# Kernel optimization log

Hardware: AMD Instinct MI355X
Metric: run time of the kernel (lower is better)

## Reference

```python
import jax, jax.numpy as jnp
import numpy as np

NEG_SLOPE = 0.2
HEADS = 8

def _gat_conv(x, src, dst, n_nodes, W, att_src, att_dst, bias):
    # x: [N, Fin], W: [Fin, H*C], att_*: [H, C], bias: [C]
    H, C = att_src.shape
    xl = (x @ W).reshape(n_nodes, H, C)                      # [N,H,C]
    a_src = (xl * att_src[None]).sum(-1)                      # [N,H]
    a_dst = (xl * att_dst[None]).sum(-1)                      # [N,H]
    e = jax.nn.leaky_relu(a_src[src] + a_dst[dst], NEG_SLOPE) # [E,H]
    m = jax.ops.segment_max(e, dst, num_segments=n_nodes)     # [N,H]
    ee = jnp.exp(e - m[dst])
    s = jax.ops.segment_sum(ee, dst, num_segments=n_nodes)    # [N,H]
    alpha = ee / s[dst]                                       # [E,H]
    msg = alpha[:, :, None] * xl[src]                         # [E,H,C]
    out = jax.ops.segment_sum(msg, dst, num_segments=n_nodes) # [N,H,C]
    return out.mean(axis=1) + bias                            # [N,C] (concat=False)

def setup_inputs() -> dict:
    key = jax.random.key(0)
    ks = jax.random.split(key, 12)
    N, E, EL = 50000, 800000, 200000
    V, D, HID, OUT = 5000, 128, 32, 32
    inp = {}
    inp['x'] = jax.random.randint(ks[0], (N,), 0, V)
    inp['edge_index'] = jax.random.randint(ks[1], (2, E), 0, N)
    inp['edge_label_index'] = jax.random.randint(ks[2], (2, EL), 0, N)
    inp['emb'] = jax.random.normal(ks[3], (V, D), jnp.float32) * D ** -0.5
    inp['W1'] = jax.random.normal(ks[4], (D, HEADS * HID), jnp.float32) * D ** -0.5
    inp['att_src1'] = jax.random.normal(ks[5], (HEADS, HID), jnp.float32) * HID ** -0.5
    inp['att_dst1'] = jax.random.normal(ks[6], (HEADS, HID), jnp.float32) * HID ** -0.5
    inp['b1'] = jnp.zeros((HID,), jnp.float32)
    inp['W2'] = jax.random.normal(ks[7], (HID, HEADS * OUT), jnp.float32) * HID ** -0.5
    inp['att_src2'] = jax.random.normal(ks[8], (HEADS, OUT), jnp.float32) * OUT ** -0.5
    inp['att_dst2'] = jax.random.normal(ks[9], (HEADS, OUT), jnp.float32) * OUT ** -0.5
    inp['b2'] = jnp.zeros((OUT,), jnp.float32)
    return inp

def reference(x, edge_index, edge_label_index, emb, W1, att_src1, att_dst1, b1, W2, att_src2, att_dst2, b2):
    N = x.shape[0]
    # PyG GATConv adds self-loops by default
    loop = jnp.arange(N)
    src = jnp.concatenate([edge_index[0], loop])
    dst = jnp.concatenate([edge_index[1], loop])
    h = emb[x]                                                   # [N, D] embedding lookup (squeeze(1) equivalent)
    h = jax.nn.relu(_gat_conv(h, src, dst, N, W1, att_src1, att_dst1, b1))
    # dropout p=0.5 is identity at inference (training=False)
    z = _gat_conv(h, src, dst, N, W2, att_src2, att_dst2, b2)    # [N, OUT]
    # decode: dot product over label edges
    return (z[edge_label_index[0]] * z[edge_label_index[1]]).sum(axis=-1)
```

## Files before the change

### kernel.cpp

```cpp
#include <hip/hip_runtime.h>
#include <hip/hip_fp16.h>
#include <math.h>
#include <limits.h>

#define HH 8
#define CC 32
#define NEG 0.2f

struct __align__(8) half4 { __half2 a, b; };

__device__ __forceinline__ int ldnt(const int* p){ return __builtin_nontemporal_load(p); }
__device__ __forceinline__ float ldntf(const float* p){ return __builtin_nontemporal_load(p); }
__device__ __forceinline__ int f2ord(float f){ int i=__float_as_int(f); return i>=0? i : i^0x7fffffff; }
__device__ __forceinline__ float ord2f(int i){ return __int_as_float(i>=0? i : i^0x7fffffff); }

__device__ __forceinline__ void edge_sd_nt(const int* __restrict__ ei, int e, int E, int& s, int& d){
  if(e < E){ s = ldnt(ei+e); d = ldnt(ei+E+e); } else { s = e-E; d = s; }
}


__global__ void k_seti(int* __restrict__ p, int n, int v){
  int i = blockIdx.x*blockDim.x + threadIdx.x;
  if(i < n) p[i] = v;
}

__global__ void k_count(const int* __restrict__ ei, int E, int ET, int* __restrict__ cnt){
  int e = blockIdx.x*blockDim.x + threadIdx.x;
  if(e >= ET) return;
  int d = (e < E) ? ldnt(ei+E+e) : e-E;
  atomicAdd(&cnt[d], 1);
}

__global__ __launch_bounds__(256) void k_scan_block(const int* __restrict__ cnt,
                                                    int* __restrict__ off,
                                                    int* __restrict__ bsum, int N){
  int i = blockIdx.x*256 + threadIdx.x;
  int v = (i < N) ? cnt[i] : 0;
  int lane = threadIdx.x & 63;
  int incl = v;
  #pragma unroll
  for(int o=1;o<64;o<<=1){ int u = __shfl_up(incl,o); if(lane>=o) incl += u; }
  __shared__ int wsum[4];
  if(lane==63) wsum[threadIdx.x>>6] = incl;
  __syncthreads();
  int w = threadIdx.x>>6, wadd = 0;
  #pragma unroll
  for(int k=0;k<4;k++) if(k<w) wadd += wsum[k];
  if(i < N) off[i] = wadd + incl - v;
  if(threadIdx.x==255) bsum[blockIdx.x] = wadd + incl;
}

__global__ __launch_bounds__(256) void k_scan_bsum(int* __restrict__ bsum, int nb,
                                                   int* __restrict__ offN){
  int t = threadIdx.x;
  int v = (t < nb) ? bsum[t] : 0;
  int lane = t & 63;
  int incl = v;
  #pragma unroll
  for(int o=1;o<64;o<<=1){ int u = __shfl_up(incl,o); if(lane>=o) incl += u; }
  __shared__ int wsum[4];
  if(lane==63) wsum[t>>6] = incl;
  __syncthreads();
  int w = t>>6, wadd = 0;
  #pragma unroll
  for(int k=0;k<4;k++) if(k<w) wadd += wsum[k];
  if(t < nb) bsum[t] = wadd + incl - v;
  if(t == 255) *offN = wadd + incl;
}

__global__ void k_scan_add(int* __restrict__ off, const int* __restrict__ bsum,
                           int* __restrict__ cur, int N){
  int i = blockIdx.x*256 + threadIdx.x;
  if(i < N){ int v = off[i] + bsum[blockIdx.x]; off[i] = v; cur[i] = v; }
}

__global__ void k_scatter(const int* __restrict__ ei, int E, int ET,
                          const int* __restrict__ x,
                          int* __restrict__ cur, int* __restrict__ csr_src,
                          int* __restrict__ csr_xv){
  int e = blockIdx.x*blockDim.x + threadIdx.x;
  if(e >= ET) return;
  int s,d; edge_sd_nt(ei,e,E,s,d);
  int pos = atomicAdd(&cur[d], 1);
  csr_src[pos] = s;
  csr_xv[pos]  = x[s];
}

__global__ __launch_bounds__(256) void k_ws(const float* __restrict__ W2,
                                            const float* __restrict__ att_s2,
                                            const float* __restrict__ att_d2,
                                            float* __restrict__ ws_s, float* __restrict__ ws_d){
  int k = threadIdx.x >> 3, h = threadIdx.x & 7;
  float ss = 0.f, dd = 0.f;
  for(int c=0;c<CC;c++){
    float w = W2[k*256 + h*CC + c];
    ss = fmaf(w, att_s2[h*CC+c], ss);
    dd = fmaf(w, att_d2[h*CC+c], dd);
  }
  ws_s[k*HH+h] = ss;
  ws_d[k*HH+h] = dd;
}

__global__ __launch_bounds__(256) void k_gmax(const float* __restrict__ a, int n8,
                                              int* __restrict__ gmax){
  int tid = blockIdx.x*256 + threadIdx.x;
  int lane = threadIdx.x & 63;
  float m = -INFINITY;
  for(int i = tid; i < n8; i += gridDim.x*256) m = fmaxf(m, a[i]);
  #pragma unroll
  for(int msk=8; msk<64; msk<<=1) m = fmaxf(m, __shfl_xor(m, msk));
  if(lane < 8) atomicMax(&gmax[lane], f2ord(m));
}

__global__ __launch_bounds__(256,4) void k_gemm1(
    const float* __restrict__ X, const float* __restrict__ W,
    const float* __restrict__ att_s, const float* __restrict__ att_d,
    __half* __restrict__ xl, float* __restrict__ a_src, float* __restrict__ a_dst, int V){
  const int ROWS = 8, FIN = 128;
  __shared__ __align__(16) float xs[ROWS][FIN];
  int row0 = blockIdx.x*ROWS;
  int tid = threadIdx.x;
  for(int p = tid; p < ROWS*FIN; p += 256){
    int r = p/FIN, kk = p - r*FIN;
    int row = row0 + r;
    xs[r][kk] = (row < V) ? ldntf(X + (size_t)row*FIN + kk) : 0.f;
  }
  __syncthreads();
  float acc[ROWS];
  #pragma unroll
  for(int r=0;r<ROWS;r++) acc[r]=0.f;
  for(int k=0;k<FIN;k++){
    float w = W[(size_t)k*256 + tid];
    #pragma unroll
    for(int r=0;r<ROWS;r++) acc[r] = fmaf(xs[r][k], w, acc[r]);
  }
  float as = att_s[tid], ad = att_d[tid];
  #pragma unroll
  for(int r=0;r<ROWS;r++){
    int n = row0+r;
    float v = acc[r];
    float ps = v*as, pd = v*ad;
    #pragma unroll
    for(int msk=16; msk>=1; msk>>=1){
      ps += __shfl_xor(ps, msk);
      pd += __shfl_xor(pd, msk);
    }
    if(n < V){
      xl[(size_t)n*256 + tid] = __float2half(v);
      if((tid&31)==0){
        int hh = tid>>5;
        a_src[n*HH+hh] = ps;
        a_dst[n*HH+hh] = pd;
      }
    }
  }
}

__global__ __launch_bounds__(256) void k_fused1(
    const int* __restrict__ off, const int* __restrict__ csr_xv,
    const int* __restrict__ x,
    const float* __restrict__ a_src_v, const float* __restrict__ a_dst_v,
    const int* __restrict__ gmax1,
    const __half* __restrict__ xl_v, const float* __restrict__ bias,
    const float* __restrict__ ws_s, const float* __restrict__ ws_d,
    __half* __restrict__ h2h, float* __restrict__ a_src2, float* __restrict__ a_dst2, int N){
  int wid = (int)((blockIdx.x*(size_t)blockDim.x + threadIdx.x) >> 6);
  int lane = threadIdx.x & 63;
  if(wid >= N) return;
  const int start = off[wid], end = off[wid+1];
  const int t = lane >> 3, h = lane & 7;
  const int xv_n = x[wid];
  const float ad = a_dst_v[xv_n*HH + h];
  float mb = ord2f(gmax1[h]) + ad;
  mb = mb > 0.f ? mb : NEG*mb;

  const int h2 = lane >> 3, c0 = (lane & 7)*4;
  const __half* xp = xl_v + h2*CC + c0;
  float eesum = 0.f;
  float4 acc = make_float4(0.f,0.f,0.f,0.f);
  for(int j0 = start; j0 < end; j0 += 8){
    int jj = j0 + t;
    int sv = 0;
    float ee = 0.f;
    if(jj < end){
      sv = ldnt(csr_xv + jj);
      float v = a_src_v[sv*HH + h] + ad;
      v = v > 0.f ? v : NEG*v;
      ee = expf(v - mb);
      eesum += ee;
    }
    #pragma unroll
    for(int u=0; u<8; ++u){
      float a  = __shfl(ee, u*8 + h2);
      int   ss = __shfl(sv, u*8);
      half4 hv = *reinterpret_cast<const half4*>(xp + (size_t)ss*256);
      float2 f01 = __half22float2(hv.a), f23 = __half22float2(hv.b);
      acc.x = fmaf(a, f01.x, acc.x);
      acc.y = fmaf(a, f01.y, acc.y);
      acc.z = fmaf(a, f23.x, acc.z);
      acc.w = fmaf(a, f23.y, acc.w);
    }
  }
  #pragma unroll
  for(int msk=8; msk<64; msk<<=1) eesum += __shfl_xor(eesum, msk);
  float is2 = 0.125f / __shfl(eesum, h2);
  acc.x *= is2; acc.y *= is2; acc.z *= is2; acc.w *= is2;
  #pragma unroll
  for(int msk=8; msk<64; msk<<=1){
    acc.x += __shfl_xor(acc.x, msk);
    acc.y += __shfl_xor(acc.y, msk);
    acc.z += __shfl_xor(acc.z, msk);
    acc.w += __shfl_xor(acc.w, msk);
  }
  if(lane < 8){
    const float4 b = *reinterpret_cast<const float4*>(bias + c0);
    float4 o = make_float4(fmaxf(acc.x+b.x,0.f), fmaxf(acc.y+b.y,0.f),
                           fmaxf(acc.z+b.z,0.f), fmaxf(acc.w+b.w,0.f));
    half4 hv;
    hv.a = __floats2half2_rn(o.x, o.y);
    hv.b = __floats2half2_rn(o.z, o.w);
    *reinterpret_cast<half4*>(h2h + (size_t)wid*CC + c0) = hv;
    float ps = 0.f, pd = 0.f;
    #pragma unroll
    for(int g=0; g<8; ++g){
      float v0 = __shfl(o.x, g), v1 = __shfl(o.y, g), v2 = __shfl(o.z, g), v3 = __shfl(o.w, g);
      int kb = g*4;
      ps = fmaf(v0, ws_s[(kb+0)*HH+lane], ps);
      ps = fmaf(v1, ws_s[(kb+1)*HH+lane], ps);
      ps = fmaf(v2, ws_s[(kb+2)*HH+lane], ps);
      ps = fmaf(v3, ws_s[(kb+3)*HH+lane], ps);
      pd = fmaf(v0, ws_d[(kb+0)*HH+lane], pd);
      pd = fmaf(v1, ws_d[(kb+1)*HH+lane], pd);
      pd = fmaf(v2, ws_d[(kb+2)*HH+lane], pd);
      pd = fmaf(v3, ws_d[(kb+3)*HH+lane], pd);
    }
    a_src2[wid*HH + lane] = ps;
    a_dst2[wid*HH + lane] = pd;
  }
}

__global__ __launch_bounds__(256) void k_fused2(
    const int* __restrict__ off, const int* __restrict__ csr_src,
    const float* __restrict__ a_src2, const float* __restrict__ a_dst2,
    const int* __restrict__ gmax2,
    const __half* __restrict__ h2h, const float* __restrict__ W2,
    const float* __restrict__ b2, float* __restrict__ z, int N){
  __shared__ __align__(16) float aggl[4][256];
  int w = threadIdx.x >> 6;
  int wid = (int)(blockIdx.x*4 + w);
  int lane = threadIdx.x & 63;
  bool active = wid < N;
  int start = 0, end = 0;
  const int t = lane >> 3, h = lane & 7;
  float ad = 0.f;
  if(active){
    start = off[wid]; end = off[wid+1];
    ad = a_dst2[wid*HH + h];
  }
  float mb = ord2f(gmax2[h]) + ad;
  mb = mb > 0.f ? mb : NEG*mb;

  const int h2 = lane >> 3, k0 = (lane & 7)*4;
  const __half* hp = h2h + k0;
  float eesum = 0.f;
  float4 acc = make_float4(0.f,0.f,0.f,0.f);
  for(int j0 = start; j0 < end; j0 += 8){
    int jj = j0 + t;
    int s = 0;
    float ee = 0.f;
    if(jj < end){
      s = ldnt(csr_src + jj);
      float v = a_src2[s*HH + h] + ad;
      v = v > 0.f ? v : NEG*v;
      ee = expf(v - mb);
      eesum += ee;
    }
    #pragma unroll
    for(int u=0; u<8; ++u){
      float a  = __shfl(ee, u*8 + h2);
      int   ss = __shfl(s,  u*8);
      half4 hv = *reinterpret_cast<const half4*>(hp + (size_t)ss*CC);
      float2 f01 = __half22float2(hv.a), f23 = __half22float2(hv.b);
      acc.x = fmaf(a, f01.x, acc.x);
      acc.y = fmaf(a, f01.y, acc.y);
      acc.z = fmaf(a, f23.x, acc.z);
      acc.w = fmaf(a, f23.y, acc.w);
    }
  }
  #pragma unroll
  for(int msk=8; msk<64; msk<<=1) eesum += __shfl_xor(eesum, msk);
  float is2 = 0.125f / __shfl(eesum, h2);
  *reinterpret_cast<float4*>(&aggl[w][h2*CC + k0]) =
      make_float4(acc.x*is2, acc.y*is2, acc.z*is2, acc.w*is2);
  __syncthreads();

  const int ch = lane & 31, part = lane >> 5;
  float p = 0.f;
  #pragma unroll
  for(int hh = 0; hh < 4; ++hh){
    int hq = part*4 + hh;
    const float* wcol = W2 + hq*CC + ch;
    const float* arow = &aggl[w][hq*CC];
    #pragma unroll 8
    for(int k=0;k<CC;k++) p = fmaf(arow[k], wcol[(size_t)k*256], p);
  }
  p += __shfl_xor(p, 32);
  if(active && part==0) z[(size_t)wid*CC + ch] = p + b2[ch];
}

__global__ void k_decode(const int* __restrict__ eli, int EL,
                         const float* __restrict__ z, float* __restrict__ out){
  int e = blockIdx.x*blockDim.x + threadIdx.x;
  if(e >= EL) return;
  const float4* za = reinterpret_cast<const float4*>(z + (size_t)ldnt(eli+e)*CC);
  const float4* zb = reinterpret_cast<const float4*>(z + (size_t)ldnt(eli+EL+e)*CC);
  float s = 0.f;
  #pragma unroll
  for(int j=0;j<8;j++){
    float4 u = za[j], v = zb[j];
    s += u.x*v.x + u.y*v.y + u.z*v.z + u.w*v.w;
  }
  out[e] = s;
}

extern "C" void kernel_launch(void* const* d_in, const int* in_sizes, int n_in,
                              void* d_out, int out_size, void* d_ws, size_t ws_size,
                              hipStream_t stream){
  const int*   x   = (const int*)d_in[0];
  const int*   ei  = (const int*)d_in[1];
  const int*   eli = (const int*)d_in[2];
  const float* emb = (const float*)d_in[3];
  const float* W1  = (const float*)d_in[4];
  const float* as1 = (const float*)d_in[5];
  const float* ad1 = (const float*)d_in[6];
  const float* b1  = (const float*)d_in[7];
  const float* W2  = (const float*)d_in[8];
  const float* as2 = (const float*)d_in[9];
  const float* ad2 = (const float*)d_in[10];
  const float* b2  = (const float*)d_in[11];

  const int N  = in_sizes[0];
  const int V  = in_sizes[3]/128;
  const int E  = in_sizes[1]/2;
  const int EL = in_sizes[2]/2;
  const int ET = E + N;

  __half* xl_v = (__half*)d_ws;
  __half* h2h  = xl_v + (size_t)V*256;
  float* a_src_v = (float*)(h2h + (size_t)N*CC);
  float* a_dst_v = a_src_v + (size_t)V*HH;
  float* a_src2  = a_dst_v + (size_t)V*HH;
  float* a_dst2  = a_src2 + (size_t)N*HH;
  float* z       = a_dst2 + (size_t)N*HH;
  float* ws_s    = z + (size_t)N*CC;
  float* ws_d    = ws_s + 256;
  int*   gmax1   = (int*)(ws_d + 256);
  int*   gmax2   = gmax1 + 8;
  int*   cnt   = gmax2 + 8;
  int*   off   = cnt + N;
  int*   cur   = off + N + 1;
  int*   bsum  = cur + N;
  int*   csr   = bsum + ((N+255)/256);
  int*   csr_xv= csr + ET;

  dim3 blk(256);
  auto cdiv = [](long long a, long long b){ return (unsigned)((a+b-1)/b); };
  const int nb = (int)cdiv(N,256);

  k_seti<<<cdiv(N,256), blk, 0, stream>>>(cnt, N, 0);
  k_seti<<<1, blk, 0, stream>>>(gmax1, 16, INT_MIN);
  k_count<<<cdiv(ET,256), blk, 0, stream>>>(ei, E, ET, cnt);
  k_scan_block<<<nb, blk, 0, stream>>>(cnt, off, bsum, N);
  k_scan_bsum<<<1, blk, 0, stream>>>(bsum, nb, off + N);
  k_scan_add<<<nb, blk, 0, stream>>>(off, bsum, cur, N);
  k_scatter<<<cdiv(ET,256), blk, 0, stream>>>(ei, E, ET, x, cur, csr, csr_xv);

  k_ws<<<1, blk, 0, stream>>>(W2, as2, ad2, ws_s, ws_d);

  k_gemm1<<<cdiv(V,8), blk, 0, stream>>>(emb, W1, as1, ad1, xl_v, a_src_v, a_dst_v, V);
  k_gmax<<<64, blk, 0, stream>>>(a_src_v, V*HH, gmax1);
  k_fused1<<<cdiv((long long)N*64,256), blk, 0, stream>>>(off, csr_xv, x, a_src_v, a_dst_v,
                                                          gmax1, xl_v, b1, ws_s, ws_d,
                                                          h2h, a_src2, a_dst2, N);

  k_gmax<<<64, blk, 0, stream>>>(a_src2, N*HH, gmax2);
  k_fused2<<<cdiv((long long)N*64,256), blk, 0, stream>>>(off, csr, a_src2, a_dst2,
                                                          gmax2, h2h, W2, b2, z, N);

  k_decode<<<cdiv(EL,256), blk, 0, stream>>>(eli, EL, z, (float*)d_out);
}
```

Before: 323.7 us.

## Prefetch edge scores, fold gmax into gemm1, split layer-2 aggregate and transform

After: 335.9 us. +3.8%, slower.

```diff
diff --git a/kernel.cpp b/kernel.cpp
--- a/kernel.cpp
+++ b/kernel.cpp
@@ -8,9 +8,12 @@
 #define NEG 0.2f
 
 struct __align__(8) half4 { __half2 a, b; };
+typedef float f32x4 __attribute__((ext_vector_type(4)));
 
 __device__ __forceinline__ int ldnt(const int* p){ return __builtin_nontemporal_load(p); }
 __device__ __forceinline__ float ldntf(const float* p){ return __builtin_nontemporal_load(p); }
+__device__ __forceinline__ f32x4 ldnt4(const float* p){ return __builtin_nontemporal_load((const f32x4*)p); }
+__device__ __forceinline__ void stnt4(float* p, f32x4 v){ __builtin_nontemporal_store(v, (f32x4*)p); }
 __device__ __forceinline__ int f2ord(float f){ int i=__float_as_int(f); return i>=0? i : i^0x7fffffff; }
 __device__ __forceinline__ float ord2f(int i){ return __int_as_float(i>=0? i : i^0x7fffffff); }
 
@@ -18,10 +21,10 @@
   if(e < E){ s = ldnt(ei+e); d = ldnt(ei+E+e); } else { s = e-E; d = s; }
 }
 
-
-__global__ void k_seti(int* __restrict__ p, int n, int v){
+__global__ void k_init2(int* __restrict__ cnt, int* __restrict__ gmax, int N){
   int i = blockIdx.x*blockDim.x + threadIdx.x;
-  if(i < n) p[i] = v;
+  if(i < N) cnt[i] = 0;
+  if(i < 16) gmax[i] = INT_MIN;
 }
 
 __global__ void k_count(const int* __restrict__ ei, int E, int ET, int* __restrict__ cnt){
@@ -115,11 +118,14 @@
 __global__ __launch_bounds__(256,4) void k_gemm1(
     const float* __restrict__ X, const float* __restrict__ W,
     const float* __restrict__ att_s, const float* __restrict__ att_d,
-    __half* __restrict__ xl, float* __restrict__ a_src, float* __restrict__ a_dst, int V){
+    __half* __restrict__ xl, float* __restrict__ a_src, float* __restrict__ a_dst,
+    int* __restrict__ gmax1, int V){
   const int ROWS = 8, FIN = 128;
   __shared__ __align__(16) float xs[ROWS][FIN];
+  __shared__ int smax[8];
   int row0 = blockIdx.x*ROWS;
   int tid = threadIdx.x;
+  if(tid < 8) smax[tid] = INT_MIN;
   for(int p = tid; p < ROWS*FIN; p += 256){
     int r = p/FIN, kk = p - r*FIN;
     int row = row0 + r;
@@ -151,9 +157,12 @@
         int hh = tid>>5;
         a_src[n*HH+hh] = ps;
         a_dst[n*HH+hh] = pd;
+        atomicMax(&smax[hh], f2ord(ps));
       }
     }
   }
+  __syncthreads();
+  if(tid < 8) atomicMax(&gmax1[tid], smax[tid]);
 }
 
 __global__ __launch_bounds__(256) void k_fused1(
@@ -176,19 +185,27 @@
 
   const int h2 = lane >> 3, c0 = (lane & 7)*4;
   const __half* xp = xl_v + h2*CC + c0;
+
+  int j0 = start;
+  int jj = j0 + t;
+  int sv = ldnt(csr_xv + min(jj, end-1));
+  float sraw = a_src_v[sv*HH + h] + ad;
+  bool valid = jj < end;
+
   float eesum = 0.f;
   float4 acc = make_float4(0.f,0.f,0.f,0.f);
-  for(int j0 = start; j0 < end; j0 += 8){
-    int jj = j0 + t;
-    int sv = 0;
-    float ee = 0.f;
-    if(jj < end){
-      sv = ldnt(csr_xv + jj);
-      float v = a_src_v[sv*HH + h] + ad;
-      v = v > 0.f ? v : NEG*v;
-      ee = expf(v - mb);
-      eesum += ee;
-    }
+  for(; j0 < end; ){
+    const int j0n = j0 + 8;
+    int svn = 0; float srawn = 0.f; bool validn = false;
+    if(j0n < end){
+      int jjn = j0n + t;
+      svn = ldnt(csr_xv + min(jjn, end-1));
+      srawn = a_src_v[svn*HH + h] + ad;
+      validn = jjn < end;
+    }
+    float v = sraw > 0.f ? sraw : NEG*sraw;
+    float ee = valid ? __expf(v - mb) : 0.f;
+    eesum += ee;
     #pragma unroll
     for(int u=0; u<8; ++u){
       float a  = __shfl(ee, u*8 + h2);
@@ -200,6 +217,7 @@
       acc.z = fmaf(a, f23.x, acc.z);
       acc.w = fmaf(a, f23.y, acc.w);
     }
+    sv = svn; sraw = srawn; valid = validn; j0 = j0n;
   }
   #pragma unroll
   for(int msk=8; msk<64; msk<<=1) eesum += __shfl_xor(eesum, msk);
@@ -239,46 +257,47 @@
   }
 }
 
-__global__ __launch_bounds__(256) void k_fused2(
+__global__ __launch_bounds__(256) void k_agg2(
     const int* __restrict__ off, const int* __restrict__ csr_src,
     const float* __restrict__ a_src2, const float* __restrict__ a_dst2,
     const int* __restrict__ gmax2,
-    const __half* __restrict__ h2h, const float* __restrict__ W2,
-    const float* __restrict__ b2, float* __restrict__ z, int N){
-  __shared__ __align__(16) float aggl[4][256];
-  int w = threadIdx.x >> 6;
-  int wid = (int)(blockIdx.x*4 + w);
+    const __half* __restrict__ h2h, float* __restrict__ agg, int N){
+  int wid = (int)((blockIdx.x*(size_t)blockDim.x + threadIdx.x) >> 6);
   int lane = threadIdx.x & 63;
-  bool active = wid < N;
-  int start = 0, end = 0;
+  if(wid >= N) return;
+  const int start = off[wid], end = off[wid+1];
   const int t = lane >> 3, h = lane & 7;
-  float ad = 0.f;
-  if(active){
-    start = off[wid]; end = off[wid+1];
-    ad = a_dst2[wid*HH + h];
-  }
+  const float ad = a_dst2[wid*HH + h];
   float mb = ord2f(gmax2[h]) + ad;
   mb = mb > 0.f ? mb : NEG*mb;
 
   const int h2 = lane >> 3, k0 = (lane & 7)*4;
   const __half* hp = h2h + k0;
+
+  int j0 = start;
+  int jj = j0 + t;
+  int sv = ldnt(csr_src + min(jj, end-1));
+  float sraw = a_src2[sv*HH + h] + ad;
+  bool valid = jj < end;
+
   float eesum = 0.f;
   float4 acc = make_float4(0.f,0.f,0.f,0.f);
-  for(int j0 = start; j0 < end; j0 += 8){
-    int jj = j0 + t;
-    int s = 0;
-    float ee = 0.f;
-    if(jj < end){
-      s = ldnt(csr_src + jj);
-      float v = a_src2[s*HH + h] + ad;
-      v = v > 0.f ? v : NEG*v;
-      ee = expf(v - mb);
-      eesum += ee;
-    }
+  for(; j0 < end; ){
+    const int j0n = j0 + 8;
+    int svn = 0; float srawn = 0.f; bool validn = false;
+    if(j0n < end){
+      int jjn = j0n + t;
+      svn = ldnt(csr_src + min(jjn, end-1));
+      srawn = a_src2[svn*HH + h] + ad;
+      validn = jjn < end;
+    }
+    float v = sraw > 0.f ? sraw : NEG*sraw;
+    float ee = valid ? __expf(v - mb) : 0.f;
+    eesum += ee;
     #pragma unroll
     for(int u=0; u<8; ++u){
       float a  = __shfl(ee, u*8 + h2);
-      int   ss = __shfl(s,  u*8);
+      int   ss = __shfl(sv, u*8);
       half4 hv = *reinterpret_cast<const half4*>(hp + (size_t)ss*CC);
       float2 f01 = __half22float2(hv.a), f23 = __half22float2(hv.b);
       acc.x = fmaf(a, f01.x, acc.x);
@@ -286,24 +305,43 @@
       acc.z = fmaf(a, f23.x, acc.z);
       acc.w = fmaf(a, f23.y, acc.w);
     }
+    sv = svn; sraw = srawn; valid = validn; j0 = j0n;
   }
   #pragma unroll
   for(int msk=8; msk<64; msk<<=1) eesum += __shfl_xor(eesum, msk);
   float is2 = 0.125f / __shfl(eesum, h2);
-  *reinterpret_cast<float4*>(&aggl[w][h2*CC + k0]) =
-      make_float4(acc.x*is2, acc.y*is2, acc.z*is2, acc.w*is2);
+  f32x4 o; o.x = acc.x*is2; o.y = acc.y*is2; o.z = acc.z*is2; o.w = acc.w*is2;
+  stnt4(agg + (size_t)wid*256 + lane*4, o);
+}
+
+__global__ __launch_bounds__(256) void k_trans2(
+    const float* __restrict__ agg, const float* __restrict__ W2,
+    const float* __restrict__ b2, float* __restrict__ z, int N){
+  __shared__ __align__(16) float aggl[4][256];
+  int w = threadIdx.x >> 6, lane = threadIdx.x & 63;
+  int wid = (int)(blockIdx.x*4 + w);
+  bool active = wid < N;
+  f32x4 av = {0.f,0.f,0.f,0.f};
+  if(active) av = ldnt4(agg + (size_t)wid*256 + lane*4);
+  *reinterpret_cast<f32x4*>(&aggl[w][lane*4]) = av;
   __syncthreads();
 
   const int ch = lane & 31, part = lane >> 5;
-  float p = 0.f;
+  float p0=0.f, p1=0.f, p2=0.f, p3=0.f;
   #pragma unroll
   for(int hh = 0; hh < 4; ++hh){
     int hq = part*4 + hh;
     const float* wcol = W2 + hq*CC + ch;
-    const float* arow = &aggl[w][hq*CC];
-    #pragma unroll 8
-    for(int k=0;k<CC;k++) p = fmaf(arow[k], wcol[(size_t)k*256], p);
-  }
+    const float* a = &aggl[w][hq*CC];
+    #pragma unroll
+    for(int k=0;k<CC;k+=4){
+      p0 = fmaf(a[k+0], wcol[(size_t)(k+0)*256], p0);
+      p1 = fmaf(a[k+1], wcol[(size_t)(k+1)*256], p1);
+      p2 = fmaf(a[k+2], wcol[(size_t)(k+2)*256], p2);
+      p3 = fmaf(a[k+3], wcol[(size_t)(k+3)*256], p3);
+    }
+  }
+  float p = (p0+p1)+(p2+p3);
   p += __shfl_xor(p, 32);
   if(active && part==0) z[(size_t)wid*CC + ch] = p + b2[ch];
 }
@@ -352,7 +390,8 @@
   float* a_src2  = a_dst_v + (size_t)V*HH;
   float* a_dst2  = a_src2 + (size_t)N*HH;
   float* z       = a_dst2 + (size_t)N*HH;
-  float* ws_s    = z + (size_t)N*CC;
+  float* agg     = z + (size_t)N*CC;
+  float* ws_s    = agg + (size_t)N*256;
   float* ws_d    = ws_s + 256;
   int*   gmax1   = (int*)(ws_d + 256);
   int*   gmax2   = gmax1 + 8;
@@ -367,8 +406,7 @@
   auto cdiv = [](long long a, long long b){ return (unsigned)((a+b-1)/b); };
   const int nb = (int)cdiv(N,256);
 
-  k_seti<<<cdiv(N,256), blk, 0, stream>>>(cnt, N, 0);
-  k_seti<<<1, blk, 0, stream>>>(gmax1, 16, INT_MIN);
+  k_init2<<<cdiv(N,256), blk, 0, stream>>>(cnt, gmax1, N);
   k_count<<<cdiv(ET,256), blk, 0, stream>>>(ei, E, ET, cnt);
   k_scan_block<<<nb, blk, 0, stream>>>(cnt, off, bsum, N);
   k_scan_bsum<<<1, blk, 0, stream>>>(bsum, nb, off + N);
@@ -377,15 +415,15 @@
 
   k_ws<<<1, blk, 0, stream>>>(W2, as2, ad2, ws_s, ws_d);
 
-  k_gemm1<<<cdiv(V,8), blk, 0, stream>>>(emb, W1, as1, ad1, xl_v, a_src_v, a_dst_v, V);
-  k_gmax<<<64, blk, 0, stream>>>(a_src_v, V*HH, gmax1);
+  k_gemm1<<<cdiv(V,8), blk, 0, stream>>>(emb, W1, as1, ad1, xl_v, a_src_v, a_dst_v, gmax1, V);
   k_fused1<<<cdiv((long long)N*64,256), blk, 0, stream>>>(off, csr_xv, x, a_src_v, a_dst_v,
                                                           gmax1, xl_v, b1, ws_s, ws_d,
                                                           h2h, a_src2, a_dst2, N);
 
   k_gmax<<<64, blk, 0, stream>>>(a_src2, N*HH, gmax2);
-  k_fused2<<<cdiv((long long)N*64,256), blk, 0, stream>>>(off, csr, a_src2, a_dst2,
-                                                          gmax2, h2h, W2, b2, z, N);
+  k_agg2<<<cdiv((long long)N*64,256), blk, 0, stream>>>(off, csr, a_src2, a_dst2,
+                                                        gmax2, h2h, agg, N);
+  k_trans2<<<cdiv(N,4), blk, 0, stream>>>(agg, W2, b2, z, N);
 
   k_decode<<<cdiv(EL,256), blk, 0, stream>>>(eli, EL, z, (float*)d_out);
 }
```
